# Optimization experiments

Hardware: AMD Instinct MI355X
Metric: run time of the kernel (lower is better)

Reference implementation:

```python
import jax, jax.numpy as jnp
import numpy as np

N, T, I, H = 64, 256, 512, 1024


def mish(x):
    return x * jnp.tanh(jax.nn.softplus(x))


def setup_inputs() -> dict:
    key = jax.random.key(0)
    ks = jax.random.split(key, 10)
    s_i = 1.0 / np.sqrt(I)
    s_h = 1.0 / np.sqrt(H)
    return {
        "x": jax.random.normal(ks[0], (N, T, I), dtype=jnp.float32),
        "is_init": jax.random.randint(ks[1], (N, T), 0, 2) > 0,
        "hx": jax.random.normal(ks[2], (N, T, H), dtype=jnp.float32),
        "cx": jax.random.normal(ks[3], (N, T, H), dtype=jnp.float32),
        "W_ih": jax.random.normal(ks[4], (4 * H, I), dtype=jnp.float32) * s_i,
        "W_hh": jax.random.normal(ks[5], (4 * H, H), dtype=jnp.float32) * s_h,
        "b_ih": jax.random.normal(ks[6], (4 * H,), dtype=jnp.float32) * s_h,
        "b_hh": jax.random.normal(ks[7], (4 * H,), dtype=jnp.float32) * s_h,
        "W_out": jax.random.normal(ks[8], (H, H), dtype=jnp.float32) * s_h,
        "b_out": jax.random.normal(ks[9], (H,), dtype=jnp.float32) * s_h,
    }


def reference(x, is_init, hx, cx, W_ih, W_hh, b_ih, b_hh, W_out, b_out):
    # recurrent_mode branch: scan LSTMCell over time with reset masking
    reset = 1.0 - is_init.astype(x.dtype)[..., None]          # [N,T,1]
    h0, c0 = hx[:, 0], cx[:, 0]                                # [N,H]

    def step(carry, inp):
        h, c = carry
        x_t, r_t = inp                                         # [N,I], [N,1]
        h = h * r_t
        c = c * r_t
        gates = x_t @ W_ih.T + b_ih + h @ W_hh.T + b_hh       # [N,4H]
        i_g, f_g, g_g, o_g = jnp.split(gates, 4, axis=-1)
        c = jax.nn.sigmoid(f_g) * c + jax.nn.sigmoid(i_g) * jnp.tanh(g_g)
        h = jax.nn.sigmoid(o_g) * jnp.tanh(c)
        return (h, c), h

    xs = (jnp.swapaxes(x, 0, 1), jnp.swapaxes(reset, 0, 1))    # time-major
    (h_f, c_f), hs = jax.lax.scan(step, (h0, c0), xs)
    hs = jnp.swapaxes(hs, 0, 1)                                # [N,T,H]
    out = mish(hs @ W_out.T + b_out)                           # Linear + Mish
    t = hs.shape[1]
    return (out,
            jnp.broadcast_to(h_f[:, None, :], (h_f.shape[0], t, h_f.shape[1])),
            jnp.broadcast_to(c_f[:, None, :], (c_f.shape[0], t, c_f.shape[1])))
```

## Files before the change

kernel.cpp:

```cpp
#include <hip/hip_runtime.h>
#include <math.h>

#define N_ 64
#define T_ 256
#define I_ 512
#define H_ 1024

typedef unsigned short u16;
typedef unsigned int u32;
typedef unsigned long long u64;
typedef short bf16x8 __attribute__((ext_vector_type(8)));
typedef float f32x4 __attribute__((ext_vector_type(4)));
typedef u16 u16x4 __attribute__((ext_vector_type(4)));
typedef u64 u64x2 __attribute__((ext_vector_type(2)));

__device__ __forceinline__ u16 f2bf(float f) {
    union { float f; unsigned int u; } x; x.f = f;
    unsigned int r = (x.u + 0x7FFFu + ((x.u >> 16) & 1u)) >> 16;
    return (u16)r;
}
__device__ __forceinline__ float bf2f(u16 u) {
    union { unsigned int u; float f; } x; x.u = ((unsigned int)u) << 16;
    return x.f;
}
__device__ __forceinline__ float sigf(float v) {
    return 1.0f / (1.0f + __expf(-v));
}
__device__ __forceinline__ float tanhfast(float x) {
    float e = __expf(2.0f * x);
    return 1.0f - 2.0f / (e + 1.0f);
}

__device__ __forceinline__ void gload_lds16n(const void* g, void* l) {
    __builtin_amdgcn_global_load_lds(
        (__attribute__((address_space(1))) void*)(g),
        (__attribute__((address_space(3))) void*)(l), 16, 0, 0);
}

#define VMW(Ncnt) do { \
    asm volatile("s_waitcnt vmcnt(" #Ncnt ")" ::: "memory"); \
    __builtin_amdgcn_sched_barrier(0); } while (0)

__device__ __forceinline__ float* c_ptr(int n, int t, int j, float* cA, float* cB) {
    return (n < 32) ? (cA + (((size_t)(n * 256 + t)) << 10) + j)
                    : (cB + (((size_t)((n - 32) * 256 + t)) << 10) + j);
}


__global__ __launch_bounds__(256) void pack_weights(
    const float* __restrict__ W_ih, const float* __restrict__ W_hh,
    const float* __restrict__ b_ih, const float* __restrict__ b_hh,
    u16* __restrict__ Wp, float* __restrict__ bp)
{
    const int rp = blockIdx.x;
    const int j = rp >> 2, g = rp & 3;
    const int src = g * H_ + j;
    const float* wi = W_ih + (size_t)src * I_;
    const float* wh = W_hh + (size_t)src * H_;
    u16* dst = Wp + (size_t)rp * (I_ + H_);
    for (int k = threadIdx.x; k < I_; k += 256) dst[k] = f2bf(wi[k]);
    for (int k = threadIdx.x; k < H_; k += 256) dst[I_ + k] = f2bf(wh[k]);
    if (threadIdx.x == 0) bp[rp] = b_ih[src] + b_hh[src];
}

__global__ __launch_bounds__(256) void conv_x(
    const float* __restrict__ x, u16* __restrict__ x_tb)
{
    const int t = blockIdx.x, n = blockIdx.y;
    const float* s = x + ((size_t)n * T_ + t) * I_;
    u16* d = x_tb + ((size_t)t * N_ + n) * I_;
    for (int k = threadIdx.x; k < I_; k += 256) d[k] = f2bf(s[k]);
}

__global__ __launch_bounds__(256) void conv_wout(
    const float* __restrict__ W, u16* __restrict__ Wb)
{
    const size_t base = (size_t)blockIdx.x * 1024 + threadIdx.x;
    #pragma unroll
    for (int q = 0; q < 4; ++q) Wb[base + q * 256] = f2bf(W[base + q * 256]);
}

__global__ __launch_bounds__(256) void conv_hx(
    const float* __restrict__ hx, u16* __restrict__ hxbf)
{
    const int idx = blockIdx.x * 256 + threadIdx.x;
    const int n = idx >> 10, j = idx & (H_ - 1);
    hxbf[idx] = f2bf(hx[(size_t)n * T_ * H_ + j]);
}

__global__ __launch_bounds__(256) void prep_rel(
    const int* __restrict__ is_init, u16* __restrict__ rel16)
{
    __shared__ u16 ii[256];
    const int n = blockIdx.x, t = threadIdx.x;
    ii[t] = (u16)(is_init[n * T_ + t] != 0);
    __syncthreads();
    int rel = t + 1;
    for (int d = 0; d <= t; ++d) {
        if (ii[t - d]) { rel = d; break; }
    }
    rel16[n * T_ + t] = (u16)rel;
}

__global__ __launch_bounds__(256) void prep_bucket(
    const u16* __restrict__ rel16, u16* __restrict__ entries, u32* __restrict__ offs)
{
    __shared__ u32 hist[258];
    __shared__ u32 offsh[258];
    const int g = blockIdx.x, tid = threadIdx.x;
    for (int i = tid; i < 258; i += 256) hist[i] = 0;
    __syncthreads();
    for (int i = tid; i < 4096; i += 256) {
        const int n = g * 16 + (i & 15), t = i >> 4;
        atomicAdd(&hist[rel16[n * T_ + t]], 1u);
    }
    __syncthreads();
    if (tid == 0) {
        u32 acc = 0;
        for (int s = 0; s < 258; ++s) { offsh[s] = acc; acc += hist[s]; }
    }
    __syncthreads();
    for (int i = tid; i < 258; i += 256) {
        offs[g * 258 + i] = offsh[i];
        hist[i] = offsh[i];
    }
    __syncthreads();
    for (int i = tid; i < 4096; i += 256) {
        const int n = g * 16 + (i & 15), t = i >> 4;
        const int rel = rel16[n * T_ + t];
        const u32 slot = atomicAdd(&hist[rel], 1u);
        entries[g * 4096 + slot] = (u16)((t << 6) | n);
    }
}

__global__ __launch_bounds__(512) __attribute__((amdgpu_waves_per_eu(2, 2)))
void xgates_mfma(
    const u16* __restrict__ x_tb,
    const u16* __restrict__ Wp,
    const float* __restrict__ bp,
    u16* __restrict__ Xg)
{
    __shared__ u16 bls[2][8192];
    const int bx = blockIdx.x, by = blockIdx.y;
    const int tid = threadIdx.x;
    const int v = tid >> 6, l = tid & 63;
    const int l15 = l & 15, lh = l >> 4;
    const int rowb = bx * 256 + v * 32;
    const int colb = by * 256;

    const u16* ap0 = x_tb + (size_t)(rowb + l15) * I_ + lh * 8;
    const u16* ap1 = x_tb + (size_t)(rowb + 16 + l15) * I_ + lh * 8;
    const u16* bs0 = Wp + (size_t)(colb + (2 * v) * 16 + l15) * 1536 + lh * 8;
    const u16* bs1 = Wp + (size_t)(colb + (2 * v + 1) * 16 + l15) * 1536 + lh * 8;

    f32x4 acc[2][16];
    #pragma unroll
    for (int m = 0; m < 2; ++m)
        #pragma unroll
        for (int nt = 0; nt < 16; ++nt) acc[m][nt] = f32x4{0.f, 0.f, 0.f, 0.f};

#define STAGEX(S, B) do { \
    gload_lds16n(bs0 + (S) * 32, (char*)bls[B] + (2 * v) * 1024); \
    gload_lds16n(bs1 + (S) * 32, (char*)bls[B] + (2 * v + 1) * 1024); } while (0)

    STAGEX(0, 0);
    VMW(0); __syncthreads();
    int buf = 0;
    for (int s = 0; s < 16; ++s) {
        if (s < 15) STAGEX(s + 1, buf ^ 1);
        bf16x8 a0 = *(const bf16x8*)(ap0 + s * 32);
        bf16x8 a1 = *(const bf16x8*)(ap1 + s * 32);
        const char* bb = (const char*)bls[buf];
        #pragma unroll
        for (int nt = 0; nt < 16; ++nt) {
            bf16x8 bfr = *(const bf16x8*)(bb + nt * 1024 + l * 16);
            acc[0][nt] = __builtin_amdgcn_mfma_f32_16x16x32_bf16(a0, bfr, acc[0][nt], 0, 0, 0);
            acc[1][nt] = __builtin_amdgcn_mfma_f32_16x16x32_bf16(a1, bfr, acc[1][nt], 0, 0, 0);
        }
        VMW(0); __syncthreads();
        buf ^= 1;
    }
#undef STAGEX

    #pragma unroll
    for (int nt = 0; nt < 16; ++nt) {
        const int col = colb + nt * 16 + l15;
        const float bo = bp[col];
        #pragma unroll
        for (int mt = 0; mt < 2; ++mt)
            #pragma unroll
            for (int rg = 0; rg < 4; ++rg) {
                const int row = rowb + mt * 16 + lh * 4 + rg;
                Xg[(size_t)row * 4096 + col] = f2bf(acc[mt][nt][rg] + bo);
            }
    }
}

__global__ __launch_bounds__(256, 1) void lstm_seg(
    const u16* __restrict__ Xg,
    const u16* __restrict__ Wp,
    const float* __restrict__ cx,
    const u16* __restrict__ hxbf,
    const u16* __restrict__ entries,
    const u32* __restrict__ offs,
    u16* __restrict__ hs,
    float* __restrict__ cA,
    float* __restrict__ cB,
    float* __restrict__ c_final,
    u32* __restrict__ flags)
{
    __shared__ u16 wls[65536];
    __shared__ u16 zls[16384];
    const int tid = threadIdx.x;
    const int v = tid >> 6, l = tid & 63;
    const int l15 = l & 15, lh = l >> 4;
    const int u = blockIdx.x & 63, g = blockIdx.x >> 6;
    const int rowbase = u * 64 + v * 16;

    {
        const u16* src = Wp + (size_t)(rowbase + l15) * 1536 + I_ + lh * 8;
        char* dst = (char*)wls + v * 32768;
        #pragma unroll
        for (int kk = 0; kk < 32; ++kk)
            gload_lds16n(src + kk * 32, dst + kk * 1024);
    }

    const int jb = u * 16 + v * 4 + lh;
    const u16* gent = entries + g * 4096;
    const u32* goff = offs + g * 258;
    u32* gflags = flags + g * 64 * 16;
    const char* wlsb = (const char*)wls + v * 32768;
    const char* zlsb = (const char*)zls;
    char* zlsw = (char*)zls;

    VMW(0);
    __syncthreads();

    {
        const int m0 = (int)goff[1];
        const int gtid = u * 256 + tid;
        for (int cell = gtid; cell < m0 * 512; cell += 64 * 256) {
            const int ri = cell >> 9, jj = cell & 511;
            const int j = jj * 2;
            const u16 e = gent[ri];
            const int t = e >> 6, n = e & 63;
            const u16* xp = Xg + ((size_t)t * 64 + n) * 4096 + 4 * j;
            const u16x4 xa = *(const u16x4*)(xp);
            const u16x4 xb = *(const u16x4*)(xp + 4);
            const float c0 = sigf(bf2f(xa[0])) * tanhfast(bf2f(xa[2]));
            const float h0 = sigf(bf2f(xa[3])) * tanhfast(c0);
            const float c1 = sigf(bf2f(xb[0])) * tanhfast(bf2f(xb[2]));
            const float h1 = sigf(bf2f(xb[3])) * tanhfast(c1);
            const size_t hrow = ((size_t)n * 256 + t) * 1024;
            __hip_atomic_store((u32*)(hs + hrow + j),
                               (u32)f2bf(h0) | ((u32)f2bf(h1) << 16),
                               __ATOMIC_RELAXED, __HIP_MEMORY_SCOPE_AGENT);
            __hip_atomic_store((u32*)c_ptr(n, t, j, cA, cB), __float_as_uint(c0),
                               __ATOMIC_RELAXED, __HIP_MEMORY_SCOPE_AGENT);
            __hip_atomic_store((u32*)c_ptr(n, t, j + 1, cA, cB), __float_as_uint(c1),
                               __ATOMIC_RELAXED, __HIP_MEMORY_SCOPE_AGENT);
            if (t == T_ - 1) {
                c_final[n * H_ + j] = c0;
                c_final[n * H_ + j + 1] = c1;
            }
        }
    }
    VMW(0);
    __syncthreads();
    if (tid == 0)
        __hip_atomic_store(gflags + u * 16, 1u,
                           __ATOMIC_RELAXED, __HIP_MEMORY_SCOPE_AGENT);
    if (tid < 64) {
        while (__hip_atomic_load(gflags + tid * 16, __ATOMIC_RELAXED,
                                 __HIP_MEMORY_SCOPE_AGENT) < 1u)
            __builtin_amdgcn_s_sleep(1);
    }
    __syncthreads();
    __builtin_amdgcn_sched_barrier(0);

    u64 rb[16];
    int nt_t = 0, nt_n = 0; bool nt_valid = false;
    float nc = 0.f; u16x4 nxg = u16x4{0, 0, 0, 0};

#define LOADT(MT, BASE, LAST) do { \
    const int ridx_ = (BASE) + (MT) * 16 + l15; \
    nt_valid = (ridx_ <= (LAST)); \
    const int cr_ = nt_valid ? ridx_ : (LAST); \
    const u16 e_ = gent[cr_]; \
    nt_t = e_ >> 6; nt_n = e_ & 63; \
    const u16* rowsrc_ = (nt_t == 0) ? (hxbf + nt_n * 1024) \
                       : (hs + ((size_t)nt_n * 256 + (nt_t - 1)) * 1024); \
    const char* lsrc_ = (const char*)rowsrc_ + lh * 16; \
    _Pragma("unroll") \
    for (int i_ = 0; i_ < 8; ++i_) { \
        const char* a_ = lsrc_ + (v * 8 + i_) * 64; \
        rb[2 * i_]     = __hip_atomic_load((const u64*)a_, \
                             __ATOMIC_RELAXED, __HIP_MEMORY_SCOPE_AGENT); \
        rb[2 * i_ + 1] = __hip_atomic_load((const u64*)(a_ + 8), \
                             __ATOMIC_RELAXED, __HIP_MEMORY_SCOPE_AGENT); \
    } \
    const float* cp_ = (nt_t == 0) ? (cx + (size_t)nt_n * T_ * H_ + jb) \
                                   : c_ptr(nt_n, nt_t - 1, jb, cA, cB); \
    nc = __uint_as_float(__hip_atomic_load((const u32*)cp_, \
                             __ATOMIC_RELAXED, __HIP_MEMORY_SCOPE_AGENT)); \
    nxg = *(const u16x4*)(Xg + ((size_t)nt_t * 64 + nt_n) * 4096 + 4 * jb); \
} while (0)

    for (int s = 1; s <= 256; ++s) {
        if (goff[s] >= 4096u) break;
        const int base = (int)goff[s];
        const int last = (int)goff[s + 1] - 1;
        const int ntiles = ((last + 1 - base) + 15) >> 4;

        LOADT(0, base, last);
        for (int mt = 0; mt < ntiles; ++mt) {
            const int cu_t = nt_t, cu_n = nt_n;
            const bool cu_valid = nt_valid;
            const float cu_c = nc;
            const u16x4 cu_xg = nxg;

            __syncthreads();
            #pragma unroll
            for (int i = 0; i < 8; ++i) {
                u64x2 w; w.x = rb[2 * i]; w.y = rb[2 * i + 1];
                *(u64x2*)(zlsw + (v * 8 + i) * 1024 + l * 16) = w;
            }
            if (mt + 1 < ntiles) LOADT(mt + 1, base, last);
            __syncthreads();

            f32x4 acc = {0.f, 0.f, 0.f, 0.f};
            #pragma unroll
            for (int kk = 0; kk < 32; ++kk) {
                bf16x8 wf = *(const bf16x8*)(wlsb + kk * 1024 + l * 16);
                bf16x8 bz = *(const bf16x8*)(zlsb + kk * 1024 + l * 16);
                acc = __builtin_amdgcn_mfma_f32_16x16x32_bf16(wf, bz, acc, 0, 0, 0);
            }

            const float ig = acc[0] + bf2f(cu_xg[0]);
            const float fg = acc[1] + bf2f(cu_xg[1]);
            const float gg = acc[2] + bf2f(cu_xg[2]);
            const float og = acc[3] + bf2f(cu_xg[3]);
            const float cn = sigf(fg) * cu_c + sigf(ig) * tanhfast(gg);
            const float hv = sigf(og) * tanhfast(cn);

            const float hvp = __shfl_down(hv, 16);
            if (cu_valid && !(lh & 1)) {
                __hip_atomic_store((u32*)(hs + ((size_t)cu_n * 256 + cu_t) * 1024 + jb),
                                   (u32)f2bf(hv) | ((u32)f2bf(hvp) << 16),
                                   __ATOMIC_RELAXED, __HIP_MEMORY_SCOPE_AGENT);
            }
            if (cu_valid) {
                __hip_atomic_store((u32*)c_ptr(cu_n, cu_t, jb, cA, cB),
                                   __float_as_uint(cn),
                                   __ATOMIC_RELAXED, __HIP_MEMORY_SCOPE_AGENT);
                if (cu_t == T_ - 1) c_final[cu_n * H_ + jb] = cn;
            }
        }

        VMW(0);
        __syncthreads();
        if (tid == 0)
            __hip_atomic_store(gflags + u * 16, (u32)(s + 1),
                               __ATOMIC_RELAXED, __HIP_MEMORY_SCOPE_AGENT);
        if (tid < 64) {
            while (__hip_atomic_load(gflags + tid * 16, __ATOMIC_RELAXED,
                                     __HIP_MEMORY_SCOPE_AGENT) < (u32)(s + 1))
                __builtin_amdgcn_s_sleep(1);
        }
        __syncthreads();
        __builtin_amdgcn_sched_barrier(0);
    }
#undef LOADT
}

__global__ __launch_bounds__(512) __attribute__((amdgpu_waves_per_eu(2, 2)))
void out_proj_mfma(
    const u16* __restrict__ hs,
    const u16* __restrict__ Wo,
    const float* __restrict__ b_out,
    float* __restrict__ out0)
{
    __shared__ u16 bls[2][8192];
    const int bx = blockIdx.x, by = blockIdx.y;
    const int tid = threadIdx.x;
    const int v = tid >> 6, l = tid & 63;
    const int l15 = l & 15, lh = l >> 4;
    const int rowb = bx * 256 + v * 32;
    const int colb = by * 256;

    const u16* ap0 = hs + (size_t)(rowb + l15) * H_ + lh * 8;
    const u16* ap1 = hs + (size_t)(rowb + 16 + l15) * H_ + lh * 8;
    const u16* bs0 = Wo + (size_t)(colb + (2 * v) * 16 + l15) * H_ + lh * 8;
    const u16* bs1 = Wo + (size_t)(colb + (2 * v + 1) * 16 + l15) * H_ + lh * 8;

    f32x4 acc[2][16];
    #pragma unroll
    for (int m = 0; m < 2; ++m)
        #pragma unroll
        for (int nt = 0; nt < 16; ++nt) acc[m][nt] = f32x4{0.f, 0.f, 0.f, 0.f};

#define STAGEO(S, B) do { \
    gload_lds16n(bs0 + (S) * 32, (char*)bls[B] + (2 * v) * 1024); \
    gload_lds16n(bs1 + (S) * 32, (char*)bls[B] + (2 * v + 1) * 1024); } while (0)

    STAGEO(0, 0);
    VMW(0); __syncthreads();
    int buf = 0;
    for (int s = 0; s < 32; ++s) {
        if (s < 31) STAGEO(s + 1, buf ^ 1);
        bf16x8 a0 = *(const bf16x8*)(ap0 + s * 32);
        bf16x8 a1 = *(const bf16x8*)(ap1 + s * 32);
        const char* bb = (const char*)bls[buf];
        #pragma unroll
        for (int nt = 0; nt < 16; ++nt) {
            bf16x8 bfr = *(const bf16x8*)(bb + nt * 1024 + l * 16);
            acc[0][nt] = __builtin_amdgcn_mfma_f32_16x16x32_bf16(a0, bfr, acc[0][nt], 0, 0, 0);
            acc[1][nt] = __builtin_amdgcn_mfma_f32_16x16x32_bf16(a1, bfr, acc[1][nt], 0, 0, 0);
        }
        VMW(0); __syncthreads();
        buf ^= 1;
    }
#undef STAGEO

    #pragma unroll
    for (int nt = 0; nt < 16; ++nt) {
        const int col = colb + nt * 16 + l15;
        const float bo = b_out[col];
        #pragma unroll
        for (int mt = 0; mt < 2; ++mt)
            #pragma unroll
            for (int rg = 0; rg < 4; ++rg) {
                const int row = rowb + mt * 16 + lh * 4 + rg;
                const float y = acc[mt][nt][rg] + bo;
                const float sp = (y > 15.f) ? y : log1pf(__expf(y));
                out0[(size_t)row * H_ + col] = y * tanhfast(sp);
            }
    }
}

__global__ __launch_bounds__(256) void bcast_h(
    const u16* __restrict__ hs, float* __restrict__ out1)
{
    const size_t total = (size_t)N_ * T_ * H_;
    for (size_t idx = (size_t)blockIdx.x * 256 + threadIdx.x; idx < total;
         idx += (size_t)gridDim.x * 256) {
        const int n = (int)(idx >> 18);
        const int j = (int)(idx & (H_ - 1));
        out1[idx] = bf2f(hs[((size_t)n * T_ + (T_ - 1)) * H_ + j]);
    }
}

__global__ __launch_bounds__(256) void bcast_c(
    const float* __restrict__ c_final, float* __restrict__ out2)
{
    const size_t total = (size_t)N_ * T_ * H_;
    for (size_t idx = (size_t)blockIdx.x * 256 + threadIdx.x; idx < total;
         idx += (size_t)gridDim.x * 256) {
        const int n = (int)(idx >> 18);
        const int j = (int)(idx & (H_ - 1));
        out2[idx] = c_final[n * H_ + j];
    }
}

extern "C" void kernel_launch(void* const* d_in, const int* in_sizes, int n_in,
                              void* d_out, int out_size, void* d_ws, size_t ws_size,
                              hipStream_t stream) {
    const float* x      = (const float*)d_in[0];
    const int*   is_ini = (const int*)  d_in[1];
    const float* hx     = (const float*)d_in[2];
    const float* cx     = (const float*)d_in[3];
    const float* W_ih   = (const float*)d_in[4];
    const float* W_hh   = (const float*)d_in[5];
    const float* b_ih   = (const float*)d_in[6];
    const float* b_hh   = (const float*)d_in[7];
    const float* W_out  = (const float*)d_in[8];
    const float* b_out  = (const float*)d_in[9];

    float* out0 = (float*)d_out;
    float* out1 = out0 + (size_t)N_ * T_ * H_;
    float* out2 = out1 + (size_t)N_ * T_ * H_;

    char* ws = (char*)d_ws;
    u16*   x_tb    = (u16*)  (ws + 0);
    u16*   Wp      = (u16*)  (ws + 16777216);
    float* bp      = (float*)(ws + 29360128);
    u16*   Wo_b    = (u16*)  (ws + 29376512);
    float* c_final = (float*)(ws + 31473664);
    u16*   hxbf    = (u16*)  (ws + 31735808);
    u16*   rel16   = (u16*)  (ws + 31866880);
    u16*   entries = (u16*)  (ws + 31899648);
    u32*   offs    = (u32*)  (ws + 31932416);
    u32*   flags   = (u32*)  (ws + 31945472);
    float* cB      = (float*)(ws + 31961856);

    u16*   Xg = (u16*)out0;
    u16*   hs = (u16*)out2;
    float* cA = (float*)(out2 + (size_t)32 * 256 * 1024);

    hipMemsetAsync(flags, 0, 16384, stream);
    pack_weights<<<4096, 256, 0, stream>>>(W_ih, W_hh, b_ih, b_hh, Wp, bp);
    conv_x<<<dim3(T_, N_), 256, 0, stream>>>(x, x_tb);
    conv_wout<<<1024, 256, 0, stream>>>(W_out, Wo_b);
    conv_hx<<<256, 256, 0, stream>>>(hx, hxbf);
    prep_rel<<<64, 256, 0, stream>>>(is_ini, rel16);
    prep_bucket<<<4, 256, 0, stream>>>(rel16, entries, offs);

    xgates_mfma<<<dim3(64, 16), 512, 0, stream>>>(x_tb, Wp, bp, Xg);

    lstm_seg<<<256, 256, 0, stream>>>(Xg, Wp, cx, hxbf, entries, offs,
                                      hs, cA, cB, c_final, flags);

    out_proj_mfma<<<dim3(64, 4), 512, 0, stream>>>(hs, Wo_b, b_out, out0);
    bcast_h<<<2048, 256, 0, stream>>>(hs, out1);
    bcast_c<<<2048, 256, 0, stream>>>(c_final, out2);
}
```

Baseline: 1.187 ms.

## Split LSTM row tiles across waves, each wave computing all four gate slices

```diff
diff --git a/kernel.cpp b/kernel.cpp
--- a/kernel.cpp
+++ b/kernel.cpp
@@ -12,7 +12,6 @@
 typedef short bf16x8 __attribute__((ext_vector_type(8)));
 typedef float f32x4 __attribute__((ext_vector_type(4)));
 typedef u16 u16x4 __attribute__((ext_vector_type(4)));
-typedef u64 u64x2 __attribute__((ext_vector_type(2)));
 
 __device__ __forceinline__ u16 f2bf(float f) {
     union { float f; unsigned int u; } x; x.f = f;
@@ -210,28 +209,23 @@
     u32* __restrict__ flags)
 {
     __shared__ u16 wls[65536];
-    __shared__ u16 zls[16384];
     const int tid = threadIdx.x;
     const int v = tid >> 6, l = tid & 63;
     const int l15 = l & 15, lh = l >> 4;
     const int u = blockIdx.x & 63, g = blockIdx.x >> 6;
-    const int rowbase = u * 64 + v * 16;
 
     {
-        const u16* src = Wp + (size_t)(rowbase + l15) * 1536 + I_ + lh * 8;
+        const u16* src = Wp + (size_t)(u * 64 + v * 16 + l15) * 1536 + I_ + lh * 8;
         char* dst = (char*)wls + v * 32768;
         #pragma unroll
         for (int kk = 0; kk < 32; ++kk)
             gload_lds16n(src + kk * 32, dst + kk * 1024);
     }
 
-    const int jb = u * 16 + v * 4 + lh;
     const u16* gent = entries + g * 4096;
     const u32* goff = offs + g * 258;
     u32* gflags = flags + g * 64 * 16;
-    const char* wlsb = (const char*)wls + v * 32768;
-    const char* zlsb = (const char*)zls;
-    char* zlsw = (char*)zls;
+    const char* wlsb = (const char*)wls;
 
     VMW(0);
     __syncthreads();
@@ -278,33 +272,7 @@
     __syncthreads();
     __builtin_amdgcn_sched_barrier(0);
 
-    u64 rb[16];
-    int nt_t = 0, nt_n = 0; bool nt_valid = false;
-    float nc = 0.f; u16x4 nxg = u16x4{0, 0, 0, 0};
-
-#define LOADT(MT, BASE, LAST) do { \
-    const int ridx_ = (BASE) + (MT) * 16 + l15; \
-    nt_valid = (ridx_ <= (LAST)); \
-    const int cr_ = nt_valid ? ridx_ : (LAST); \
-    const u16 e_ = gent[cr_]; \
-    nt_t = e_ >> 6; nt_n = e_ & 63; \
-    const u16* rowsrc_ = (nt_t == 0) ? (hxbf + nt_n * 1024) \
-                       : (hs + ((size_t)nt_n * 256 + (nt_t - 1)) * 1024); \
-    const char* lsrc_ = (const char*)rowsrc_ + lh * 16; \
-    _Pragma("unroll") \
-    for (int i_ = 0; i_ < 8; ++i_) { \
-        const char* a_ = lsrc_ + (v * 8 + i_) * 64; \
-        rb[2 * i_]     = __hip_atomic_load((const u64*)a_, \
-                             __ATOMIC_RELAXED, __HIP_MEMORY_SCOPE_AGENT); \
-        rb[2 * i_ + 1] = __hip_atomic_load((const u64*)(a_ + 8), \
-                             __ATOMIC_RELAXED, __HIP_MEMORY_SCOPE_AGENT); \
-    } \
-    const float* cp_ = (nt_t == 0) ? (cx + (size_t)nt_n * T_ * H_ + jb) \
-                                   : c_ptr(nt_n, nt_t - 1, jb, cA, cB); \
-    nc = __uint_as_float(__hip_atomic_load((const u32*)cp_, \
-                             __ATOMIC_RELAXED, __HIP_MEMORY_SCOPE_AGENT)); \
-    nxg = *(const u16x4*)(Xg + ((size_t)nt_t * 64 + nt_n) * 4096 + 4 * jb); \
-} while (0)
+    union AU { u64 q[2]; bf16x8 b; };
 
     for (int s = 1; s <= 256; ++s) {
         if (goff[s] >= 4096u) break;
@@ -312,48 +280,70 @@
         const int last = (int)goff[s + 1] - 1;
         const int ntiles = ((last + 1 - base) + 15) >> 4;
 
-        LOADT(0, base, last);
-        for (int mt = 0; mt < ntiles; ++mt) {
-            const int cu_t = nt_t, cu_n = nt_n;
-            const bool cu_valid = nt_valid;
-            const float cu_c = nc;
-            const u16x4 cu_xg = nxg;
-
-            __syncthreads();
-            #pragma unroll
-            for (int i = 0; i < 8; ++i) {
-                u64x2 w; w.x = rb[2 * i]; w.y = rb[2 * i + 1];
-                *(u64x2*)(zlsw + (v * 8 + i) * 1024 + l * 16) = w;
-            }
-            if (mt + 1 < ntiles) LOADT(mt + 1, base, last);
-            __syncthreads();
-
-            f32x4 acc = {0.f, 0.f, 0.f, 0.f};
+        for (int mt = v; mt < ntiles; mt += 4) {
+            const int ridx = base + mt * 16 + l15;
+            const bool valid = (ridx <= last);
+            const u16 e = gent[valid ? ridx : last];
+            const int t = e >> 6, n = e & 63;
+
+            const u16* rowsrc = (t == 0) ? (hxbf + n * 1024)
+                               : (hs + ((size_t)n * 256 + (t - 1)) * 1024);
+            const char* lsrc = (const char*)rowsrc + lh * 16;
+            AU a[32];
             #pragma unroll
             for (int kk = 0; kk < 32; ++kk) {
-                bf16x8 wf = *(const bf16x8*)(wlsb + kk * 1024 + l * 16);
-                bf16x8 bz = *(const bf16x8*)(zlsb + kk * 1024 + l * 16);
-                acc = __builtin_amdgcn_mfma_f32_16x16x32_bf16(wf, bz, acc, 0, 0, 0);
-            }
-
-            const float ig = acc[0] + bf2f(cu_xg[0]);
-            const float fg = acc[1] + bf2f(cu_xg[1]);
-            const float gg = acc[2] + bf2f(cu_xg[2]);
-            const float og = acc[3] + bf2f(cu_xg[3]);
-            const float cn = sigf(fg) * cu_c + sigf(ig) * tanhfast(gg);
-            const float hv = sigf(og) * tanhfast(cn);
-
-            const float hvp = __shfl_down(hv, 16);
-            if (cu_valid && !(lh & 1)) {
-                __hip_atomic_store((u32*)(hs + ((size_t)cu_n * 256 + cu_t) * 1024 + jb),
-                                   (u32)f2bf(hv) | ((u32)f2bf(hvp) << 16),
-                                   __ATOMIC_RELAXED, __HIP_MEMORY_SCOPE_AGENT);
-            }
-            if (cu_valid) {
-                __hip_atomic_store((u32*)c_ptr(cu_n, cu_t, jb, cA, cB),
-                                   __float_as_uint(cn),
-                                   __ATOMIC_RELAXED, __HIP_MEMORY_SCOPE_AGENT);
-                if (cu_t == T_ - 1) c_final[cu_n * H_ + jb] = cn;
+                a[kk].q[0] = __hip_atomic_load((const u64*)(lsrc + kk * 64),
+                                 __ATOMIC_RELAXED, __HIP_MEMORY_SCOPE_AGENT);
+                a[kk].q[1] = __hip_atomic_load((const u64*)(lsrc + kk * 64 + 8),
+                                 __ATOMIC_RELAXED, __HIP_MEMORY_SCOPE_AGENT);
+            }
+
+            const u16* xrow = Xg + ((size_t)t * 64 + n) * 4096;
+            u16x4 xg[4]; float cprev[4];
+            #pragma unroll
+            for (int q = 0; q < 4; ++q) {
+                const int jbq = u * 16 + q * 4 + lh;
+                xg[q] = *(const u16x4*)(xrow + 4 * jbq);
+                const float* cp = (t == 0) ? (cx + (size_t)n * T_ * H_ + jbq)
+                                           : c_ptr(n, t - 1, jbq, cA, cB);
+                cprev[q] = __uint_as_float(__hip_atomic_load((const u32*)cp,
+                               __ATOMIC_RELAXED, __HIP_MEMORY_SCOPE_AGENT));
+            }
+
+            f32x4 acc[4];
+            #pragma unroll
+            for (int q = 0; q < 4; ++q) acc[q] = f32x4{0.f, 0.f, 0.f, 0.f};
+            #pragma unroll
+            for (int q = 0; q < 4; ++q) {
+                #pragma unroll
+                for (int kk = 0; kk < 32; ++kk) {
+                    bf16x8 wf = *(const bf16x8*)(wlsb + q * 32768 + kk * 1024 + l * 16);
+                    acc[q] = __builtin_amdgcn_mfma_f32_16x16x32_bf16(wf, a[kk].b, acc[q], 0, 0, 0);
+                }
+            }
+
+            #pragma unroll
+            for (int q = 0; q < 4; ++q) {
+                const int jbq = u * 16 + q * 4 + lh;
+                const float ig = acc[q][0] + bf2f(xg[q][0]);
+                const float fg = acc[q][1] + bf2f(xg[q][1]);
+                const float gg = acc[q][2] + bf2f(xg[q][2]);
+                const float og = acc[q][3] + bf2f(xg[q][3]);
+                const float cn = sigf(fg) * cprev[q] + sigf(ig) * tanhfast(gg);
+                const float hv = sigf(og) * tanhfast(cn);
+
+                const float hvp = __shfl_down(hv, 16);
+                if (valid && !(lh & 1)) {
+                    __hip_atomic_store((u32*)(hs + ((size_t)n * 256 + t) * 1024 + jbq),
+                                       (u32)f2bf(hv) | ((u32)f2bf(hvp) << 16),
+                                       __ATOMIC_RELAXED, __HIP_MEMORY_SCOPE_AGENT);
+                }
+                if (valid) {
+                    __hip_atomic_store((u32*)c_ptr(n, t, jbq, cA, cB),
+                                       __float_as_uint(cn),
+                                       __ATOMIC_RELAXED, __HIP_MEMORY_SCOPE_AGENT);
+                    if (t == T_ - 1) c_final[n * H_ + jbq] = cn;
+                }
             }
         }
 
@@ -370,7 +360,6 @@
         __syncthreads();
         __builtin_amdgcn_sched_barrier(0);
     }
-#undef LOADT
 }
 
 __global__ __launch_bounds__(512) __attribute__((amdgpu_waves_per_eu(2, 2)))
```

Result: no change. 1.185 ms (-0.2%).
